# Optimization experiments

Measured on AMD Instinct MI355X. Metric: run time of the kernel, lower is better.

Reference implementation:

```python
import jax, jax.numpy as jnp
import numpy as np

B, T, D, H = 4, 2048, 1024, 16
HD = D // H  # head_dim = 64

def setup_inputs() -> dict:
    key = jax.random.key(0)
    k1, k2, k3 = jax.random.split(key, 3)
    scale_in = 1.0 / np.sqrt(D)
    return {
        "x": jax.random.normal(k1, (B, T, D), dtype=jnp.float32),
        "W_qkv": jax.random.normal(k2, (D, 3 * D), dtype=jnp.float32) * scale_in,
        "b_qkv": jnp.zeros((3 * D,), dtype=jnp.float32),
        "W_out": jax.random.normal(k3, (D, D), dtype=jnp.float32) * scale_in,
        "b_out": jnp.zeros((D,), dtype=jnp.float32),
    }

def reference(x, W_qkv, b_qkv, W_out, b_out):
    Bx, Tx, C = x.shape
    qkv = x @ W_qkv + b_qkv                      # [B,T,3D]
    q, k, v = jnp.split(qkv, 3, axis=-1)
    # [B,T,D] -> [B,H,T,hd]
    def to_heads(t):
        return t.reshape(Bx, Tx, H, HD).transpose(0, 2, 1, 3)
    q, k, v = to_heads(q), to_heads(k), to_heads(v)
    scores = jnp.einsum('bhqd,bhkd->bhqk', q, k) / np.sqrt(HD)  # [B,H,T,T]
    causal = jnp.tril(jnp.ones((Tx, Tx), dtype=bool))
    scores = jnp.where(causal, scores, -jnp.inf)
    attn = jax.nn.softmax(scores, axis=-1)       # dropout p=0 -> identity
    out = jnp.einsum('bhqk,bhkd->bhqd', attn, v)  # [B,H,T,hd]
    out = out.transpose(0, 2, 1, 3).reshape(Bx, Tx, C)
    return out @ W_out + b_out
```

## Files before the change

### kernel.cpp

```cpp
#include <hip/hip_runtime.h>
#include <hip/hip_bf16.h>

#define BB 4
#define TT 2048
#define DD 1024
#define HH 16
#define HDIM 64
#define BT (BB*TT)
#define D3 (3*DD)

typedef __attribute__((ext_vector_type(8))) short bf16x8;
typedef __attribute__((ext_vector_type(4))) float f32x4;

#if __has_builtin(__builtin_amdgcn_exp2f)
#define EXP2(x) __builtin_amdgcn_exp2f(x)
#else
#define EXP2(x) exp2f(x)
#endif

__device__ __forceinline__ ushort f2bf(float f) {
  union { float f; uint32_t u; } v; v.f = f;
  uint32_t u = v.u + 0x7FFFu + ((v.u >> 16) & 1u);
  return (ushort)(u >> 16);
}

__device__ __forceinline__ ushort f2bf_hw(float f) {
  __hip_bfloat16 h = __float2bfloat16(f);
  ushort u;
  __builtin_memcpy(&u, &h, 2);
  return u;
}

__device__ __forceinline__ float bf2f(ushort u) {
  union { uint32_t i; float f; } x; x.i = ((uint32_t)u) << 16; return x.f;
}

__device__ __forceinline__ void gload_lds16(const void* g, void* l) {
  __builtin_amdgcn_global_load_lds((const __attribute__((address_space(1))) void*)g,
                                   (__attribute__((address_space(3))) void*)l, 16, 0, 0);
}

__global__ __launch_bounds__(256)
void cvt_bf16(const float* __restrict__ in, ushort* __restrict__ out, int n4) {
  int i = blockIdx.x * blockDim.x + threadIdx.x;
  int stride = gridDim.x * blockDim.x;
  for (; i < n4; i += stride) {
    float4 v = ((const float4*)in)[i];
    ushort4 o;
    o.x = f2bf(v.x); o.y = f2bf(v.y); o.z = f2bf(v.z); o.w = f2bf(v.w);
    ((ushort4*)out)[i] = o;
  }
}

__global__ __launch_bounds__(256)
void transpose_cvt(const float* __restrict__ W, ushort* __restrict__ Wt, int K, int N) {
  __shared__ ushort Tt[64][68];
  const int n0 = blockIdx.x * 64;
  const int k0 = blockIdx.y * 64;
  const int tid = threadIdx.x;
  const int r = tid >> 4;
  const int c4 = (tid & 15) * 4;
  #pragma unroll
  for (int i = 0; i < 4; ++i) {
    int row = r + i * 16;
    float4 v = *(const float4*)&W[(size_t)(k0 + row) * N + n0 + c4];
    Tt[c4 + 0][row] = f2bf(v.x);
    Tt[c4 + 1][row] = f2bf(v.y);
    Tt[c4 + 2][row] = f2bf(v.z);
    Tt[c4 + 3][row] = f2bf(v.w);
  }
  __syncthreads();
  #pragma unroll
  for (int i = 0; i < 4; ++i) {
    int row = r + i * 16;
    ushort4 tv = *(const ushort4*)&Tt[row][c4];
    *(ushort4*)&Wt[(size_t)(n0 + row) * K + k0 + c4] = tv;
  }
}

template<bool F32OUT>
__global__ __launch_bounds__(256)
void gemm_bt(const ushort* __restrict__ A, const ushort* __restrict__ Bw,
             const float* __restrict__ bias, void* __restrict__ C, int N) {
  __shared__ __align__(16) short As[128 * 64];
  __shared__ __align__(16) short Bs[128 * 64];
  const int tid = threadIdx.x;
  const int w = tid >> 6, lane = tid & 63;
  const int li = lane & 15, g = lane >> 4;
  const int wm = w >> 1, wn = w & 1;
  const int bm = blockIdx.y * 128;
  const int bn = blockIdx.x * 128;
  const int lrow = lane >> 3;
  const int lchunk = lane & 7;

  f32x4 acc[4][4] = {};

  for (int k0 = 0; k0 < 1024; k0 += 64) {
    __syncthreads();
    #pragma unroll
    for (int j = 0; j < 4; ++j) {
      int row = j * 32 + w * 8 + lrow;
      gload_lds16(A  + (size_t)(bm + row) * 1024 + k0 + lchunk * 8, As + j * 2048 + w * 512);
      gload_lds16(Bw + (size_t)(bn + row) * 1024 + k0 + lchunk * 8, Bs + j * 2048 + w * 512);
    }
    __syncthreads();
    #pragma unroll
    for (int c = 0; c < 2; ++c) {
      bf16x8 af[4], bfr[4];
      #pragma unroll
      for (int mi = 0; mi < 4; ++mi)
        af[mi] = *(bf16x8*)&As[(wm * 64 + mi * 16 + li) * 64 + c * 32 + g * 8];
      #pragma unroll
      for (int ni = 0; ni < 4; ++ni)
        bfr[ni] = *(bf16x8*)&Bs[(wn * 64 + ni * 16 + li) * 64 + c * 32 + g * 8];
      #pragma unroll
      for (int mi = 0; mi < 4; ++mi)
        #pragma unroll
        for (int ni = 0; ni < 4; ++ni)
          acc[mi][ni] = __builtin_amdgcn_mfma_f32_16x16x32_bf16(af[mi], bfr[ni], acc[mi][ni], 0, 0, 0);
    }
  }
  #pragma unroll
  for (int ni = 0; ni < 4; ++ni) {
    int col = bn + wn * 64 + ni * 16 + li;
    float bv = bias[col];
    #pragma unroll
    for (int mi = 0; mi < 4; ++mi) {
      int row = bm + wm * 64 + mi * 16 + g * 4;
      #pragma unroll
      for (int r = 0; r < 4; ++r) {
        float v = acc[mi][ni][r] + bv;
        if (F32OUT) ((float*)C)[(size_t)(row + r) * N + col] = v;
        else        ((ushort*)C)[(size_t)(row + r) * N + col] = f2bf_hw(v);
      }
    }
  }
}

__global__ __launch_bounds__(512, 2)
void gemm_qkv_8p(const ushort* __restrict__ A, const ushort* __restrict__ Bw,
                 const float* __restrict__ bias, ushort* __restrict__ C, int N) {
  __shared__ __align__(16) short lds[4 * 256 * 64];

  const int tid = threadIdx.x;
  const int w = tid >> 6;
  const int wm = w >> 2;
  const int wn = w & 3;
  const int lane = tid & 63;
  const int li = lane & 15, g = lane >> 4;
  const int swz = (li & 7) << 4;

  const int bm = blockIdx.y * 256;
  const int bn = blockIdx.x * 256;
  const ushort* Ag = A + (size_t)bm * 1024;
  const ushort* Bg = Bw + (size_t)bn * 1024;

  const int lrow8 = lane >> 3;
  const int chsw = (lane & 7) ^ lrow8;

  f32x4 acc[8][4] = {};

#define STAGE8(t, p) do { \
  const int kk_ = (t) * 64; \
  short* Ad_ = lds + (p) * 32768; \
  short* Bd_ = Ad_ + 16384; \
  _Pragma("unroll") \
  for (int h_ = 0; h_ < 2; ++h_) { \
    _Pragma("unroll") \
    for (int j_ = 0; j_ < 2; ++j_) { \
      const int r_ = h_ * 128 + w * 16 + j_ * 8; \
      gload_lds16(Ag + (size_t)(r_ + lrow8) * 1024 + kk_ + chsw * 8, Ad_ + r_ * 64); \
      gload_lds16(Bg + (size_t)(r_ + lrow8) * 1024 + kk_ + chsw * 8, Bd_ + r_ * 64); \
    } \
  } \
} while (0)

  STAGE8(0, 0);
  asm volatile("s_waitcnt vmcnt(0)" ::: "memory");
  __builtin_amdgcn_sched_barrier(0);
  __builtin_amdgcn_s_barrier();

  for (int s = 0; s < 16; ++s) {
    const int cur = s & 1;
    const char* Ab = (const char*)lds + cur * 65536;
    const char* Bb = Ab + 32768;

    if (s + 1 < 16) STAGE8(s + 1, cur ^ 1);

    bf16x8 af[8], bf[4];
    #pragma unroll
    for (int mi = 0; mi < 8; ++mi)
      af[mi] = *(const bf16x8*)(Ab + (wm * 128 + mi * 16 + li) * 128 + ((g * 16) ^ swz));
    #pragma unroll
    for (int ni = 0; ni < 2; ++ni)
      bf[ni] = *(const bf16x8*)(Bb + (wn * 64 + ni * 16 + li) * 128 + ((g * 16) ^ swz));
    __builtin_amdgcn_s_setprio(1);
    #pragma unroll
    for (int mi = 0; mi < 8; ++mi)
      #pragma unroll
      for (int ni = 0; ni < 2; ++ni)
        acc[mi][ni] = __builtin_amdgcn_mfma_f32_16x16x32_bf16(af[mi], bf[ni], acc[mi][ni], 0, 0, 0);
    __builtin_amdgcn_s_setprio(0);
    __builtin_amdgcn_s_barrier();
    #pragma unroll
    for (int ni = 2; ni < 4; ++ni)
      bf[ni] = *(const bf16x8*)(Bb + (wn * 64 + ni * 16 + li) * 128 + ((g * 16) ^ swz));
    __builtin_amdgcn_s_setprio(1);
    #pragma unroll
    for (int mi = 0; mi < 8; ++mi)
      #pragma unroll
      for (int ni = 2; ni < 4; ++ni)
        acc[mi][ni] = __builtin_amdgcn_mfma_f32_16x16x32_bf16(af[mi], bf[ni], acc[mi][ni], 0, 0, 0);
    __builtin_amdgcn_s_setprio(0);
    __builtin_amdgcn_s_barrier();
    #pragma unroll
    for (int mi = 0; mi < 8; ++mi)
      af[mi] = *(const bf16x8*)(Ab + (wm * 128 + mi * 16 + li) * 128 + ((64 + g * 16) ^ swz));
    #pragma unroll
    for (int ni = 0; ni < 2; ++ni)
      bf[ni] = *(const bf16x8*)(Bb + (wn * 64 + ni * 16 + li) * 128 + ((64 + g * 16) ^ swz));
    __builtin_amdgcn_s_setprio(1);
    #pragma unroll
    for (int mi = 0; mi < 8; ++mi)
      #pragma unroll
      for (int ni = 0; ni < 2; ++ni)
        acc[mi][ni] = __builtin_amdgcn_mfma_f32_16x16x32_bf16(af[mi], bf[ni], acc[mi][ni], 0, 0, 0);
    __builtin_amdgcn_s_setprio(0);
    __builtin_amdgcn_s_barrier();
    #pragma unroll
    for (int ni = 2; ni < 4; ++ni)
      bf[ni] = *(const bf16x8*)(Bb + (wn * 64 + ni * 16 + li) * 128 + ((64 + g * 16) ^ swz));
    __builtin_amdgcn_s_setprio(1);
    #pragma unroll
    for (int mi = 0; mi < 8; ++mi)
      #pragma unroll
      for (int ni = 2; ni < 4; ++ni)
        acc[mi][ni] = __builtin_amdgcn_mfma_f32_16x16x32_bf16(af[mi], bf[ni], acc[mi][ni], 0, 0, 0);
    __builtin_amdgcn_s_setprio(0);
    asm volatile("s_waitcnt vmcnt(0)" ::: "memory");
    __builtin_amdgcn_sched_barrier(0);
    __builtin_amdgcn_s_barrier();
  }
#undef STAGE8

  #pragma unroll
  for (int ni = 0; ni < 4; ++ni) {
    int col = bn + wn * 64 + ni * 16 + li;
    float bv = bias[col];
    #pragma unroll
    for (int mi = 0; mi < 8; ++mi) {
      int row = bm + wm * 128 + mi * 16 + g * 4;
      #pragma unroll
      for (int r = 0; r < 4; ++r)
        C[(size_t)(row + r) * N + col] = f2bf_hw(acc[mi][ni][r] + bv);
    }
  }
}

__global__ void zero_ctr(uint* c) { *c = 0u; }

#define NITEMS 1024

__global__ __launch_bounds__(256)
void attn_mfma(const ushort* __restrict__ qkv, ushort* __restrict__ out,
               uint* __restrict__ ctr) {
  __shared__ __align__(16) short Ks[64 * 64];
  __shared__ __align__(16) short Vt[64 * 64];
  __shared__ __align__(16) short Pl[4 * 16 * 64];
  __shared__ int s_item;

  const int tid = threadIdx.x;
  const int w = tid >> 6;
  const int lane = tid & 63;
  const int li = lane & 15, g = lane >> 4;
  const int sw = (li & 7) << 4;

  char* KsB = (char*)Ks;
  char* VtB = (char*)Vt;
  char* PlB = (char*)Pl + w * 2048;

  const int krow0 = tid >> 3;
  const int kc = tid & 7;
  const int d0 = (tid >> 5) * 8;
  const int kp = tid & 31;
  const int kswz = (kc * 16) ^ ((krow0 & 7) << 4);

  for (;;) {
    if (tid == 0) s_item = (int)atomicAdd(ctr, 1u);
    __syncthreads();
    const int item = s_item;
    if (item >= NITEMS) return;

    const int qt = 15 - (item >> 6);
    const int bh = item & 63;
    const int h = bh & 15, b = bh >> 4;
    const int qg0 = qt * 128 + w * 32;

    bf16x8 qfr[2][2];
    #pragma unroll
    for (int qf = 0; qf < 2; ++qf) {
      const ushort* qrow = qkv + (size_t)(b * TT + qg0 + qf * 16 + li) * D3 + h * HDIM;
      #pragma unroll
      for (int c = 0; c < 2; ++c) {
        uint4 raw = *(const uint4*)(qrow + c * 32 + g * 8);
        const ushort* rp = (const ushort*)&raw;
        bf16x8 v;
        #pragma unroll
        for (int j = 0; j < 8; ++j)
          v[j] = (short)f2bf_hw(bf2f(rp[j]) * 0.18033688f);
        qfr[qf][c] = v;
      }
    }

    f32x4 o[4][2] = {};
    float lsum[2] = {0.f, 0.f};

    const ushort* kbase = qkv + (size_t)b * TT * D3 + DD + h * HDIM;
    const ushort* vbase = kbase + DD;

    const int nt = 2 * qt + 2;
    const int itlast = 2 * qt + (w >> 1);

    uint4 kpre0, kpre1, vpre0, vpre1;
    {
      const ushort* kg = kbase + (size_t)krow0 * D3 + kc * 8;
      kpre0 = *(const uint4*)kg;
      kpre1 = *(const uint4*)(kg + (size_t)32 * D3);
      const ushort* vg = vbase + (size_t)(2 * kp) * D3 + d0;
      vpre0 = *(const uint4*)vg;
      vpre1 = *(const uint4*)(vg + D3);
    }

    for (int it = 0; it < nt; ++it) {
      const int k0 = it * 64;
      *(uint4*)(KsB + krow0 * 128 + kswz) = kpre0;
      *(uint4*)(KsB + (krow0 + 32) * 128 + kswz) = kpre1;
      {
        const ushort* pa = (const ushort*)&vpre0;
        const ushort* pb = (const ushort*)&vpre1;
        #pragma unroll
        for (int j = 0; j < 8; ++j) {
          uint32_t pk = (uint32_t)pa[j] | ((uint32_t)pb[j] << 16);
          *(uint32_t*)(VtB + (d0 + j) * 128 + ((4 * kp) ^ (j << 4))) = pk;
        }
      }
      __syncthreads();
      if (it + 1 < nt) {
        const ushort* kg = kbase + (size_t)(k0 + 64 + krow0) * D3 + kc * 8;
        kpre0 = *(const uint4*)kg;
        kpre1 = *(const uint4*)(kg + (size_t)32 * D3);
        const ushort* vg = vbase + (size_t)(k0 + 64 + 2 * kp) * D3 + d0;
        vpre0 = *(const uint4*)vg;
        vpre1 = *(const uint4*)(vg + D3);
      }
      if (it <= itlast) {
        const bool domask = (it == itlast);
        bf16x8 pf[2][2];
        f32x4 s[2][4];
        __builtin_amdgcn_s_setprio(1);
        #pragma unroll
        for (int kt = 0; kt < 4; ++kt) {
          const int row = kt * 16 + li;
          bf16x8 kf0 = *(bf16x8*)(KsB + row * 128 + ((g * 16) ^ sw));
          bf16x8 kf1 = *(bf16x8*)(KsB + row * 128 + ((64 + g * 16) ^ sw));
          #pragma unroll
          for (int qf = 0; qf < 2; ++qf) {
            f32x4 a = {0.f, 0.f, 0.f, 0.f};
            a = __builtin_amdgcn_mfma_f32_16x16x32_bf16(kf0, qfr[qf][0], a, 0, 0, 0);
            a = __builtin_amdgcn_mfma_f32_16x16x32_bf16(kf1, qfr[qf][1], a, 0, 0, 0);
            s[qf][kt] = a;
          }
        }
        __builtin_amdgcn_s_setprio(0);
        #pragma unroll
        for (int qf = 0; qf < 2; ++qf) {
          const int qrow = qg0 + qf * 16 + li;
          if (domask) {
            #pragma unroll
            for (int kt = 0; kt < 4; ++kt)
              #pragma unroll
              for (int r = 0; r < 4; ++r) {
                int key = k0 + kt * 16 + g * 4 + r;
                if (key > qrow) s[qf][kt][r] = -1e30f;
              }
          }
          float ls = 0.f;
          #pragma unroll
          for (int kt = 0; kt < 4; ++kt) {
            float p0 = EXP2(s[qf][kt][0]);
            float p1 = EXP2(s[qf][kt][1]);
            float p2 = EXP2(s[qf][kt][2]);
            float p3 = EXP2(s[qf][kt][3]);
            ls += (p0 + p1) + (p2 + p3);
            uint2 val;
            val.x = (uint32_t)f2bf_hw(p0) | ((uint32_t)f2bf_hw(p1) << 16);
            val.y = (uint32_t)f2bf_hw(p2) | ((uint32_t)f2bf_hw(p3) << 16);
            *(uint2*)(PlB + li * 128 + ((kt * 32 + g * 8) ^ sw)) = val;
          }
          lsum[qf] += ls;
          pf[qf][0] = *(bf16x8*)(PlB + li * 128 + ((g * 16) ^ sw));
          pf[qf][1] = *(bf16x8*)(PlB + li * 128 + ((64 + g * 16) ^ sw));
        }
        __builtin_amdgcn_s_setprio(1);
        #pragma unroll
        for (int dt = 0; dt < 4; ++dt) {
          const int vrow = dt * 16 + li;
          bf16x8 vf0 = *(bf16x8*)(VtB + vrow * 128 + ((g * 16) ^ sw));
          bf16x8 vf1 = *(bf16x8*)(VtB + vrow * 128 + ((64 + g * 16) ^ sw));
          #pragma unroll
          for (int qf = 0; qf < 2; ++qf) {
            o[dt][qf] = __builtin_amdgcn_mfma_f32_16x16x32_bf16(vf0, pf[qf][0], o[dt][qf], 0, 0, 0);
            o[dt][qf] = __builtin_amdgcn_mfma_f32_16x16x32_bf16(vf1, pf[qf][1], o[dt][qf], 0, 0, 0);
          }
        }
        __builtin_amdgcn_s_setprio(0);
      }
      __syncthreads();
    }

    #pragma unroll
    for (int qf = 0; qf < 2; ++qf) {
      float lt = lsum[qf];
      lt += __shfl_xor(lt, 16);
      lt += __shfl_xor(lt, 32);
      float inv = 1.f / lt;
      ushort* orow = out + (size_t)(b * TT + qg0 + qf * 16 + li) * DD + h * HDIM;
      #pragma unroll
      for (int dt = 0; dt < 4; ++dt) {
        uint2 pk;
        pk.x = (uint32_t)f2bf_hw(o[dt][qf][0] * inv) | ((uint32_t)f2bf_hw(o[dt][qf][1] * inv) << 16);
        pk.y = (uint32_t)f2bf_hw(o[dt][qf][2] * inv) | ((uint32_t)f2bf_hw(o[dt][qf][3] * inv) << 16);
        *(uint2*)&orow[dt * 16 + g * 4] = pk;
      }
    }
  }
}

extern "C" void kernel_launch(void* const* d_in, const int* in_sizes, int n_in,
                              void* d_out, int out_size, void* d_ws, size_t ws_size,
                              hipStream_t stream) {
  const float* x     = (const float*)d_in[0];
  const float* W_qkv = (const float*)d_in[1];
  const float* b_qkv = (const float*)d_in[2];
  const float* W_out = (const float*)d_in[3];
  const float* b_out = (const float*)d_in[4];
  float* out = (float*)d_out;

  ushort* x_bf   = (ushort*)d_ws;
  ushort* wtq    = x_bf + (size_t)BT * DD;
  ushort* wto    = wtq + (size_t)D3 * DD;
  ushort* qkv_bf = wto + (size_t)DD * DD;
  ushort* att_bf = qkv_bf + (size_t)BT * D3;
  uint*   ctr    = (uint*)(att_bf + (size_t)BT * DD);

  zero_ctr<<<1, 1, 0, stream>>>(ctr);
  cvt_bf16<<<2048, 256, 0, stream>>>(x, x_bf, BT * DD / 4);
  transpose_cvt<<<dim3(D3 / 64, DD / 64), 256, 0, stream>>>(W_qkv, wtq, DD, D3);
  transpose_cvt<<<dim3(DD / 64, DD / 64), 256, 0, stream>>>(W_out, wto, DD, DD);

  gemm_qkv_8p<<<dim3(D3 / 256, BT / 256), 512, 0, stream>>>(x_bf, wtq, b_qkv, qkv_bf, D3);
  attn_mfma<<<dim3(1024), 256, 0, stream>>>(qkv_bf, att_bf, ctr);
  gemm_bt<true><<<dim3(DD / 128, BT / 128), 256, 0, stream>>>(att_bf, wto, b_out, (void*)out, DD);
}
```

Before: 192.0 us.

## Split long causal query tiles across two KV chunks and add combine kernel

Query tiles 8–15 are now split into two work items that each cover half of the key range, ordered interleaved with the short tiles. This shrinks the longest work items and reduces tail imbalance in the persistent attention scheduler. The partial unnormalized outputs and row sums are written in bf16/fp32 to a scratch slab that reuses the dead x_bf buffer, and a new combine kernel merges them. Separately, the counter reset moves into the conversion kernel to drop one launch. The cost is extra global traffic, one extra kernel, and rounding the partial sums to bf16 before they are combined.

```diff
diff --git a/kernel.cpp b/kernel.cpp
--- a/kernel.cpp
+++ b/kernel.cpp
@@ -41,7 +41,9 @@
 }
 
 __global__ __launch_bounds__(256)
-void cvt_bf16(const float* __restrict__ in, ushort* __restrict__ out, int n4) {
+void cvt_bf16(const float* __restrict__ in, ushort* __restrict__ out, int n4,
+              uint* __restrict__ ctr) {
+  if (blockIdx.x == 0 && threadIdx.x == 0) *ctr = 0u;
   int i = blockIdx.x * blockDim.x + threadIdx.x;
   int stride = gridDim.x * blockDim.x;
   for (; i < n4; i += stride) {
@@ -257,13 +259,12 @@
   }
 }
 
-__global__ void zero_ctr(uint* c) { *c = 0u; }
-
-#define NITEMS 1024
+#define NITEMS 1536
+#define PSTRIDE 8448
 
 __global__ __launch_bounds__(256)
 void attn_mfma(const ushort* __restrict__ qkv, ushort* __restrict__ out,
-               uint* __restrict__ ctr) {
+               uint* __restrict__ ctr, ushort* __restrict__ pslab) {
   __shared__ __align__(16) short Ks[64 * 64];
   __shared__ __align__(16) short Vt[64 * 64];
   __shared__ __align__(16) short Pl[4 * 16 * 64];
@@ -291,8 +292,41 @@
     const int item = s_item;
     if (item >= NITEMS) return;
 
-    const int qt = 15 - (item >> 6);
-    const int bh = item & 63;
+    int qt, base, sp;
+    if      (item < 128)  { base = 0;    qt = 15; sp = 1; }
+    else if (item < 192)  { base = 128;  qt = 7;  sp = 0; }
+    else if (item < 320)  { base = 192;  qt = 14; sp = 1; }
+    else if (item < 448)  { base = 320;  qt = 13; sp = 1; }
+    else if (item < 512)  { base = 448;  qt = 6;  sp = 0; }
+    else if (item < 640)  { base = 512;  qt = 12; sp = 1; }
+    else if (item < 768)  { base = 640;  qt = 11; sp = 1; }
+    else if (item < 832)  { base = 768;  qt = 5;  sp = 0; }
+    else if (item < 960)  { base = 832;  qt = 10; sp = 1; }
+    else if (item < 1088) { base = 960;  qt = 9;  sp = 1; }
+    else if (item < 1152) { base = 1088; qt = 4;  sp = 0; }
+    else if (item < 1280) { base = 1152; qt = 8;  sp = 1; }
+    else if (item < 1344) { base = 1280; qt = 3;  sp = 0; }
+    else if (item < 1408) { base = 1344; qt = 2;  sp = 0; }
+    else if (item < 1472) { base = 1408; qt = 1;  sp = 0; }
+    else                  { base = 1472; qt = 0;  sp = 0; }
+    const int local = item - base;
+    int bh, kstart, ntt, slot;
+    bool nomask;
+    if (sp) {
+      const int chunk = local >> 6;
+      bh = local & 63;
+      kstart = chunk ? (qt + 1) : 0;
+      ntt = qt + 1;
+      nomask = (chunk == 0);
+      slot = ((qt - 8) * 64 + bh) * 2 + chunk;
+    } else {
+      bh = local & 63;
+      kstart = 0;
+      ntt = 2 * qt + 2;
+      nomask = false;
+      slot = -1;
+    }
+
     const int h = bh & 15, b = bh >> 4;
     const int qg0 = qt * 128 + w * 32;
 
@@ -318,21 +352,20 @@
     const ushort* kbase = qkv + (size_t)b * TT * D3 + DD + h * HDIM;
     const ushort* vbase = kbase + DD;
 
-    const int nt = 2 * qt + 2;
-    const int itlast = 2 * qt + (w >> 1);
+    const int itlast = nomask ? (ntt - 1) : (ntt - 2 + (w >> 1));
 
     uint4 kpre0, kpre1, vpre0, vpre1;
     {
-      const ushort* kg = kbase + (size_t)krow0 * D3 + kc * 8;
+      const ushort* kg = kbase + (size_t)(kstart * 64 + krow0) * D3 + kc * 8;
       kpre0 = *(const uint4*)kg;
       kpre1 = *(const uint4*)(kg + (size_t)32 * D3);
-      const ushort* vg = vbase + (size_t)(2 * kp) * D3 + d0;
+      const ushort* vg = vbase + (size_t)(kstart * 64 + 2 * kp) * D3 + d0;
       vpre0 = *(const uint4*)vg;
       vpre1 = *(const uint4*)(vg + D3);
     }
 
-    for (int it = 0; it < nt; ++it) {
-      const int k0 = it * 64;
+    for (int it = 0; it < ntt; ++it) {
+      const int k0 = (kstart + it) * 64;
       *(uint4*)(KsB + krow0 * 128 + kswz) = kpre0;
       *(uint4*)(KsB + (krow0 + 32) * 128 + kswz) = kpre1;
       {
@@ -345,7 +378,7 @@
         }
       }
       __syncthreads();
-      if (it + 1 < nt) {
+      if (it + 1 < ntt) {
         const ushort* kg = kbase + (size_t)(k0 + 64 + krow0) * D3 + kc * 8;
         kpre0 = *(const uint4*)kg;
         kpre1 = *(const uint4*)(kg + (size_t)32 * D3);
@@ -354,7 +387,7 @@
         vpre1 = *(const uint4*)(vg + D3);
       }
       if (it <= itlast) {
-        const bool domask = (it == itlast);
+        const bool domask = (!nomask) && (it == itlast);
         bf16x8 pf[2][2];
         f32x4 s[2][4];
         __builtin_amdgcn_s_setprio(1);
@@ -418,21 +451,69 @@
       __syncthreads();
     }
 
-    #pragma unroll
-    for (int qf = 0; qf < 2; ++qf) {
-      float lt = lsum[qf];
-      lt += __shfl_xor(lt, 16);
-      lt += __shfl_xor(lt, 32);
-      float inv = 1.f / lt;
-      ushort* orow = out + (size_t)(b * TT + qg0 + qf * 16 + li) * DD + h * HDIM;
-      #pragma unroll
-      for (int dt = 0; dt < 4; ++dt) {
-        uint2 pk;
-        pk.x = (uint32_t)f2bf_hw(o[dt][qf][0] * inv) | ((uint32_t)f2bf_hw(o[dt][qf][1] * inv) << 16);
-        pk.y = (uint32_t)f2bf_hw(o[dt][qf][2] * inv) | ((uint32_t)f2bf_hw(o[dt][qf][3] * inv) << 16);
-        *(uint2*)&orow[dt * 16 + g * 4] = pk;
-      }
-    }
+    if (slot >= 0) {
+      ushort* ps = pslab + (size_t)slot * PSTRIDE;
+      #pragma unroll
+      for (int qf = 0; qf < 2; ++qf) {
+        float lt = lsum[qf];
+        lt += __shfl_xor(lt, 16);
+        lt += __shfl_xor(lt, 32);
+        const int q = w * 32 + qf * 16 + li;
+        #pragma unroll
+        for (int dt = 0; dt < 4; ++dt) {
+          uint2 pk;
+          pk.x = (uint32_t)f2bf_hw(o[dt][qf][0]) | ((uint32_t)f2bf_hw(o[dt][qf][1]) << 16);
+          pk.y = (uint32_t)f2bf_hw(o[dt][qf][2]) | ((uint32_t)f2bf_hw(o[dt][qf][3]) << 16);
+          *(uint2*)&ps[q * 64 + dt * 16 + g * 4] = pk;
+        }
+        if (g == 0) ((float*)(ps + 8192))[q] = lt;
+      }
+    } else {
+      #pragma unroll
+      for (int qf = 0; qf < 2; ++qf) {
+        float lt = lsum[qf];
+        lt += __shfl_xor(lt, 16);
+        lt += __shfl_xor(lt, 32);
+        float inv = 1.f / lt;
+        ushort* orow = out + (size_t)(b * TT + qg0 + qf * 16 + li) * DD + h * HDIM;
+        #pragma unroll
+        for (int dt = 0; dt < 4; ++dt) {
+          uint2 pk;
+          pk.x = (uint32_t)f2bf_hw(o[dt][qf][0] * inv) | ((uint32_t)f2bf_hw(o[dt][qf][1] * inv) << 16);
+          pk.y = (uint32_t)f2bf_hw(o[dt][qf][2] * inv) | ((uint32_t)f2bf_hw(o[dt][qf][3] * inv) << 16);
+          *(uint2*)&orow[dt * 16 + g * 4] = pk;
+        }
+      }
+    }
+  }
+}
+
+__global__ __launch_bounds__(256)
+void combine_attn(const ushort* __restrict__ pslab, ushort* __restrict__ out) {
+  const int bid = blockIdx.x;
+  const int qt = 8 + (bid >> 6);
+  const int bh = bid & 63;
+  const int h = bh & 15, b = bh >> 4;
+  const ushort* pA = pslab + (size_t)(((qt - 8) * 64 + bh) * 2) * PSTRIDE;
+  const ushort* pB = pA + PSTRIDE;
+  const float* lA = (const float*)(pA + 8192);
+  const float* lB = (const float*)(pB + 8192);
+  const int t = threadIdx.x;
+  #pragma unroll
+  for (int i = 0; i < 8; ++i) {
+    int idx = t + i * 256;
+    int q = idx >> 4, dc = idx & 15;
+    float inv = 1.f / (lA[q] + lB[q]);
+    uint2 a  = *(const uint2*)&pA[q * 64 + dc * 4];
+    uint2 b2 = *(const uint2*)&pB[q * 64 + dc * 4];
+    float v0 = (bf2f((ushort)(a.x & 0xffff)) + bf2f((ushort)(b2.x & 0xffff))) * inv;
+    float v1 = (bf2f((ushort)(a.x >> 16))    + bf2f((ushort)(b2.x >> 16)))    * inv;
+    float v2 = (bf2f((ushort)(a.y & 0xffff)) + bf2f((ushort)(b2.y & 0xffff))) * inv;
+    float v3 = (bf2f((ushort)(a.y >> 16))    + bf2f((ushort)(b2.y >> 16)))    * inv;
+    uint2 r;
+    r.x = (uint32_t)f2bf_hw(v0) | ((uint32_t)f2bf_hw(v1) << 16);
+    r.y = (uint32_t)f2bf_hw(v2) | ((uint32_t)f2bf_hw(v3) << 16);
+    *(uint2*)&out[(size_t)(b * TT + qt * 128 + q) * DD + h * HDIM + dc * 4] = r;
   }
 }
 
@@ -452,13 +533,14 @@
   ushort* qkv_bf = wto + (size_t)DD * DD;
   ushort* att_bf = qkv_bf + (size_t)BT * D3;
   uint*   ctr    = (uint*)(att_bf + (size_t)BT * DD);
-
-  zero_ctr<<<1, 1, 0, stream>>>(ctr);
-  cvt_bf16<<<2048, 256, 0, stream>>>(x, x_bf, BT * DD / 4);
+  ushort* pslab  = x_bf;
+
+  cvt_bf16<<<2048, 256, 0, stream>>>(x, x_bf, BT * DD / 4, ctr);
   transpose_cvt<<<dim3(D3 / 64, DD / 64), 256, 0, stream>>>(W_qkv, wtq, DD, D3);
   transpose_cvt<<<dim3(DD / 64, DD / 64), 256, 0, stream>>>(W_out, wto, DD, DD);
 
   gemm_qkv_8p<<<dim3(D3 / 256, BT / 256), 512, 0, stream>>>(x_bf, wtq, b_qkv, qkv_bf, D3);
-  attn_mfma<<<dim3(1024), 256, 0, stream>>>(qkv_bf, att_bf, ctr);
+  attn_mfma<<<dim3(1024), 256, 0, stream>>>(qkv_bf, att_bf, ctr, pslab);
+  combine_attn<<<dim3(512), 256, 0, stream>>>(pslab, att_bf);
   gemm_bt<true><<<dim3(DD / 128, BT / 128), 256, 0, stream>>>(att_bf, wto, b_out, (void*)out, DD);
 }
```

Measured after the change: 193.9 us. Within noise of the previous version (+1.0%).

## Double-buffer K tiles via direct global-to-LDS loads and fold counter reset

Applied to the files above, without the earlier changes.

The attention kernel now loads K tiles straight into a double-buffered LDS array with global_load_lds, replacing the register-staged prefetch and LDS store. This frees registers and store instructions, and the next K tile can load while the current one is consumed. Explicit vmcnt waits with sched barriers are added before the block barriers in attention and in the output GEMM so the async LDS loads finish first. The separate counter-zeroing launch is folded into the conversion kernel, removing one kernel launch. The swizzle changes from XOR on the LDS address to XOR on the global column chunk.

```diff
diff --git a/kernel.cpp b/kernel.cpp
--- a/kernel.cpp
+++ b/kernel.cpp
@@ -41,7 +41,9 @@
 }
 
 __global__ __launch_bounds__(256)
-void cvt_bf16(const float* __restrict__ in, ushort* __restrict__ out, int n4) {
+void cvt_bf16(const float* __restrict__ in, ushort* __restrict__ out, int n4,
+              uint* __restrict__ ctr) {
+  if (blockIdx.x == 0 && threadIdx.x == 0) *ctr = 0u;
   int i = blockIdx.x * blockDim.x + threadIdx.x;
   int stride = gridDim.x * blockDim.x;
   for (; i < n4; i += stride) {
@@ -103,6 +105,8 @@
       gload_lds16(A  + (size_t)(bm + row) * 1024 + k0 + lchunk * 8, As + j * 2048 + w * 512);
       gload_lds16(Bw + (size_t)(bn + row) * 1024 + k0 + lchunk * 8, Bs + j * 2048 + w * 512);
     }
+    asm volatile("s_waitcnt vmcnt(0)" ::: "memory");
+    __builtin_amdgcn_sched_barrier(0);
     __syncthreads();
     #pragma unroll
     for (int c = 0; c < 2; ++c) {
@@ -257,14 +261,12 @@
   }
 }
 
-__global__ void zero_ctr(uint* c) { *c = 0u; }
-
 #define NITEMS 1024
 
 __global__ __launch_bounds__(256)
 void attn_mfma(const ushort* __restrict__ qkv, ushort* __restrict__ out,
                uint* __restrict__ ctr) {
-  __shared__ __align__(16) short Ks[64 * 64];
+  __shared__ __align__(16) short Ks[2][64 * 64];
   __shared__ __align__(16) short Vt[64 * 64];
   __shared__ __align__(16) short Pl[4 * 16 * 64];
   __shared__ int s_item;
@@ -275,15 +277,14 @@
   const int li = lane & 15, g = lane >> 4;
   const int sw = (li & 7) << 4;
 
-  char* KsB = (char*)Ks;
   char* VtB = (char*)Vt;
   char* PlB = (char*)Pl + w * 2048;
 
-  const int krow0 = tid >> 3;
-  const int kc = tid & 7;
+  const int lrow = lane >> 3;
+  const int lsw = ((lane & 7) ^ lrow) * 8;
+
   const int d0 = (tid >> 5) * 8;
   const int kp = tid & 31;
-  const int kswz = (kc * 16) ^ ((krow0 & 7) << 4);
 
   for (;;) {
     if (tid == 0) s_item = (int)atomicAdd(ctr, 1u);
@@ -296,6 +297,26 @@
     const int h = bh & 15, b = bh >> 4;
     const int qg0 = qt * 128 + w * 32;
 
+    const ushort* kbase = qkv + (size_t)b * TT * D3 + DD + h * HDIM;
+    const ushort* vbase = kbase + DD;
+
+#define KSTAGE(t, buf) do { \
+  const ushort* kg_ = kbase + (size_t)(t) * 64 * D3 + lsw; \
+  _Pragma("unroll") \
+  for (int i_ = 0; i_ < 2; ++i_) { \
+    const int row_ = i_ * 32 + w * 8 + lrow; \
+    gload_lds16(kg_ + (size_t)row_ * D3, &Ks[buf][(i_ * 256 + w * 64) * 8]); \
+  } \
+} while (0)
+
+    KSTAGE(0, 0);
+    uint4 vpre0, vpre1;
+    {
+      const ushort* vg = vbase + (size_t)(2 * kp) * D3 + d0;
+      vpre0 = *(const uint4*)vg;
+      vpre1 = *(const uint4*)(vg + D3);
+    }
+
     bf16x8 qfr[2][2];
     #pragma unroll
     for (int qf = 0; qf < 2; ++qf) {
@@ -315,26 +336,11 @@
     f32x4 o[4][2] = {};
     float lsum[2] = {0.f, 0.f};
 
-    const ushort* kbase = qkv + (size_t)b * TT * D3 + DD + h * HDIM;
-    const ushort* vbase = kbase + DD;
-
-    const int nt = 2 * qt + 2;
+    const int ntt = 2 * qt + 2;
     const int itlast = 2 * qt + (w >> 1);
 
-    uint4 kpre0, kpre1, vpre0, vpre1;
-    {
-      const ushort* kg = kbase + (size_t)krow0 * D3 + kc * 8;
-      kpre0 = *(const uint4*)kg;
-      kpre1 = *(const uint4*)(kg + (size_t)32 * D3);
-      const ushort* vg = vbase + (size_t)(2 * kp) * D3 + d0;
-      vpre0 = *(const uint4*)vg;
-      vpre1 = *(const uint4*)(vg + D3);
-    }
-
-    for (int it = 0; it < nt; ++it) {
+    for (int it = 0; it < ntt; ++it) {
       const int k0 = it * 64;
-      *(uint4*)(KsB + krow0 * 128 + kswz) = kpre0;
-      *(uint4*)(KsB + (krow0 + 32) * 128 + kswz) = kpre1;
       {
         const ushort* pa = (const ushort*)&vpre0;
         const ushort* pb = (const ushort*)&vpre1;
@@ -344,17 +350,18 @@
           *(uint32_t*)(VtB + (d0 + j) * 128 + ((4 * kp) ^ (j << 4))) = pk;
         }
       }
+      asm volatile("s_waitcnt vmcnt(0)" ::: "memory");
+      __builtin_amdgcn_sched_barrier(0);
       __syncthreads();
-      if (it + 1 < nt) {
-        const ushort* kg = kbase + (size_t)(k0 + 64 + krow0) * D3 + kc * 8;
-        kpre0 = *(const uint4*)kg;
-        kpre1 = *(const uint4*)(kg + (size_t)32 * D3);
+      if (it + 1 < ntt) {
+        KSTAGE(it + 1, (it + 1) & 1);
         const ushort* vg = vbase + (size_t)(k0 + 64 + 2 * kp) * D3 + d0;
         vpre0 = *(const uint4*)vg;
         vpre1 = *(const uint4*)(vg + D3);
       }
       if (it <= itlast) {
         const bool domask = (it == itlast);
+        const char* KsB = (const char*)Ks + (it & 1) * 8192;
         bf16x8 pf[2][2];
         f32x4 s[2][4];
         __builtin_amdgcn_s_setprio(1);
@@ -417,6 +424,7 @@
       }
       __syncthreads();
     }
+#undef KSTAGE
 
     #pragma unroll
     for (int qf = 0; qf < 2; ++qf) {
@@ -453,8 +461,7 @@
   ushort* att_bf = qkv_bf + (size_t)BT * D3;
   uint*   ctr    = (uint*)(att_bf + (size_t)BT * DD);
 
-  zero_ctr<<<1, 1, 0, stream>>>(ctr);
-  cvt_bf16<<<2048, 256, 0, stream>>>(x, x_bf, BT * DD / 4);
+  cvt_bf16<<<2048, 256, 0, stream>>>(x, x_bf, BT * DD / 4, ctr);
   transpose_cvt<<<dim3(D3 / 64, DD / 64), 256, 0, stream>>>(W_qkv, wtq, DD, D3);
   transpose_cvt<<<dim3(DD / 64, DD / 64), 256, 0, stream>>>(W_out, wto, DD, DD);
 
```

Result: no change. 193.0 us (+0.5%).
